# Kernel tuning notes

Measured on AMD Instinct MI355X. Metric: run time of the kernel, lower is better.

## Reference

```python
import jax, jax.numpy as jnp
import numpy as np

D_MODEL = 1024
NUM_SYMBOLS = 1024
NUM_VALUES = 1024
GRAPH_STEPS = 3
BATCH = 64


def setup_inputs() -> dict:
    key = jax.random.key(0)
    ks = jax.random.split(key, 12)
    B, S, V, D = BATCH, NUM_SYMBOLS, NUM_VALUES, D_MODEL
    scale = 0.02
    return {
        "map_memory": jax.random.normal(ks[0], (B, S, V), jnp.float32) * scale,
        "step_memory": jax.random.normal(ks[1], (B, S, S), jnp.float32) * scale,
        "query_idx": jax.random.randint(ks[2], (B,), 0, S),
        "query_mask": jnp.ones((B,), jnp.float32),
        "symbol_bank": jax.random.normal(ks[3], (S, D), jnp.float32) * scale,
        "value_bank": jax.random.normal(ks[4], (V, D), jnp.float32) * scale,
        "Wo1": jax.random.normal(ks[5], (D, D), jnp.float32) * scale,
        "bo1": jnp.zeros((D,), jnp.float32),
        "Wo2": jax.random.normal(ks[6], (D, V), jnp.float32) * scale,
        "bo2": jnp.zeros((V,), jnp.float32),
        "Wf1": jax.random.normal(ks[7], (D, D), jnp.float32) * scale,
        "bf1": jnp.zeros((D,), jnp.float32),
        "Wf2": jax.random.normal(ks[8], (D, D), jnp.float32) * scale,
        "bf2": jnp.zeros((D,), jnp.float32),
    }


def reference(map_memory, step_memory, query_idx, query_mask,
              symbol_bank, value_bank,
              Wo1, bo1, Wo2, bo2, Wf1, bf1, Wf2, bf2):
    # query_state: [B, S] one-hot masked
    query_state = jax.nn.one_hot(query_idx, NUM_SYMBOLS, dtype=jnp.float32)
    query_state = query_state * query_mask[:, None]

    acc_values = jnp.einsum('bs,bsv->bv', query_state, map_memory)   # [B, V]
    acc_symbols = jnp.einsum('bs,sd->bd', query_state, symbol_bank)  # [B, D]

    def walk_step(carry, _):
        walk, values, symbols = carry
        next_walk = jnp.einsum('bs,bst->bt', walk, step_memory)
        next_values = values + jnp.einsum('bs,bsv->bv', next_walk, map_memory)
        next_symbols = symbols + jnp.einsum('bs,sd->bd', next_walk, symbol_bank)
        return (next_walk, next_values, next_symbols), None

    (_, acc_values, acc_symbols), _ = jax.lax.scan(
        walk_step, (query_state, acc_values, acc_symbols), xs=None,
        length=GRAPH_STEPS)

    graph_state = acc_symbols + jnp.einsum('bv,vd->bd', acc_values, value_bank)

    logits = jax.nn.gelu(graph_state @ Wo1 + bo1) @ Wo2 + bo2      # [B, V]
    feedback = jax.nn.gelu(graph_state @ Wf1 + bf1) @ Wf2 + bf2    # [B, D]
    return logits, feedback
```

## Files before the change

### kernel.cpp

```cpp
#include <hip/hip_runtime.h>

#define BB 64
#define SS 1024
#define NN 1024
#define PARTS 16
#define KC 64

typedef float f4 __attribute__((ext_vector_type(4)));

template<int ASRC, int REV, int NT>
__global__ __launch_bounds__(256) void k_walkp(const float* __restrict__ A,
                                               const float* __restrict__ P,
                                               const float* __restrict__ W,
                                               float* __restrict__ Cp,
                                               const int* __restrict__ qidx,
                                               const float* __restrict__ qmask) {
    const int part = blockIdx.x;
    const int b    = REV ? (gridDim.y - 1 - blockIdx.y) : blockIdx.y;
    const int k0   = part * KC;

    __shared__ float As[KC];
    if (threadIdx.x < KC) {
        float v;
        if (ASRC == 0) {
            int q = qidx[b];
            v = qmask[b] * W[(size_t)b * SS * SS + (size_t)q * SS + k0 + threadIdx.x];
        } else if (ASRC == 1) {
            v = 0.f;
            #pragma unroll
            for (int p = 0; p < PARTS; ++p)
                v += P[(size_t)p * BB * SS + b * SS + k0 + threadIdx.x];
        } else {
            v = A[b * SS + k0 + threadIdx.x];
        }
        As[threadIdx.x] = v;
    }
    __syncthreads();

    const float* Wp = W + (size_t)b * SS * SS + (size_t)k0 * NN + threadIdx.x * 4;
    f4 acc = {0.f, 0.f, 0.f, 0.f};
    for (int k = 0; k < KC; ++k) {
        f4 wv;
        if (NT) wv = __builtin_nontemporal_load((const f4*)(Wp + (size_t)k * NN));
        else    wv = *(const f4*)(Wp + (size_t)k * NN);
        float a = As[k];
        acc.x = fmaf(a, wv.x, acc.x);
        acc.y = fmaf(a, wv.y, acc.y);
        acc.z = fmaf(a, wv.z, acc.z);
        acc.w = fmaf(a, wv.w, acc.w);
    }
    f4* c = (f4*)(Cp + (size_t)part * BB * SS + (size_t)b * SS) + threadIdx.x;
    *c = acc;
}

__global__ void k_wsum(const float* __restrict__ SM,
                       const float* __restrict__ P,
                       const int* __restrict__ qidx, const float* __restrict__ qmask,
                       float* __restrict__ Wsum) {
    int b = blockIdx.x;
    int q = qidx[b];
    float m = qmask[b];
    int s0 = threadIdx.x * 4;

    f4 acc = m * (*(const f4*)(SM + (size_t)b * SS * SS + (size_t)q * SS + s0));
    #pragma unroll
    for (int p = 0; p < 2 * PARTS; ++p)
        acc += *(const f4*)(P + (size_t)p * BB * SS + b * SS + s0);
    int d = q - s0;
    if (d >= 0 && d < 4) acc[d] += m;
    *(f4*)(Wsum + b * SS + s0) = acc;
}

template<int ROWS, int KCS, int AR0, int AR1>
__global__ __launch_bounds__(256) void k_small(const float* __restrict__ A0,
                                               const float* __restrict__ W0,
                                               float* __restrict__ C0,
                                               const float* __restrict__ A1,
                                               const float* __restrict__ W1,
                                               float* __restrict__ C1,
                                               const float* __restrict__ P) {
    const int   ar = blockIdx.z ? AR1 : AR0;
    const float* A = blockIdx.z ? A1 : A0;
    const float* W = blockIdx.z ? W1 : W0;
    float*       C = blockIdx.z ? C1 : C0;
    const int k0 = blockIdx.x * KCS;
    const int r0 = blockIdx.y * ROWS;

    __shared__ float As[ROWS * KCS];
    for (int i = threadIdx.x; i < ROWS * KCS; i += 256) {
        int r = i / KCS, k = i % KCS;
        float v;
        if (ar) {
            v = 0.f;
            #pragma unroll
            for (int p = 0; p < PARTS; ++p)
                v += P[(size_t)p * BB * SS + (size_t)(r0 + r) * SS + k0 + k];
        } else {
            v = A[(r0 + r) * NN + k0 + k];
        }
        As[i] = v;
    }
    __syncthreads();

    const float* Wp = W + (size_t)k0 * NN + threadIdx.x * 4;
    float acc[ROWS][4];
    #pragma unroll
    for (int r = 0; r < ROWS; ++r) {
        acc[r][0] = 0.f; acc[r][1] = 0.f; acc[r][2] = 0.f; acc[r][3] = 0.f;
    }
    for (int k = 0; k < KCS; ++k) {
        float4 wv = *(const float4*)(Wp + (size_t)k * NN);
        #pragma unroll
        for (int r = 0; r < ROWS; ++r) {
            float a = As[r * KCS + k];
            acc[r][0] = fmaf(a, wv.x, acc[r][0]);
            acc[r][1] = fmaf(a, wv.y, acc[r][1]);
            acc[r][2] = fmaf(a, wv.z, acc[r][2]);
            acc[r][3] = fmaf(a, wv.w, acc[r][3]);
        }
    }
    const int t = threadIdx.x * 4;
    #pragma unroll
    for (int r = 0; r < ROWS; ++r) {
        float* c = C + (size_t)(r0 + r) * NN + t;
        unsafeAtomicAdd(c + 0, acc[r][0]);
        unsafeAtomicAdd(c + 1, acc[r][1]);
        unsafeAtomicAdd(c + 2, acc[r][2]);
        unsafeAtomicAdd(c + 3, acc[r][3]);
    }
}

__global__ void k_biasgelu(float* __restrict__ h0, float* __restrict__ h1,
                           const float* __restrict__ b0, const float* __restrict__ b1) {
    float* h = blockIdx.y ? h1 : h0;
    const float* bias = blockIdx.y ? b1 : b0;
    int b = blockIdx.x;
    int t = threadIdx.x * 4;
    #pragma unroll
    for (int j = 0; j < 4; ++j) {
        int d = t + j;
        float x = h[b * NN + d] + bias[d];
        float c = 0.7978845608028654f * (x + 0.044715f * x * x * x);
        h[b * NN + d] = 0.5f * x * (1.0f + tanhf(c));
    }
}

__global__ void k_out(const float* __restrict__ lg, const float* __restrict__ fb,
                      const float* __restrict__ bo2, const float* __restrict__ bf2,
                      float* __restrict__ out) {
    int half = blockIdx.y;
    const float* src = half ? fb : lg;
    const float* bias = half ? bf2 : bo2;
    float* dst = out + (size_t)half * BB * NN;
    int b = blockIdx.x;
    int t = threadIdx.x * 4;
    #pragma unroll
    for (int j = 0; j < 4; ++j) {
        int n = t + j;
        dst[b * NN + n] = src[b * NN + n] + bias[n];
    }
}

extern "C" void kernel_launch(void* const* d_in, const int* in_sizes, int n_in,
                              void* d_out, int out_size, void* d_ws, size_t ws_size,
                              hipStream_t stream) {
    const float* MM   = (const float*)d_in[0];
    const float* SM   = (const float*)d_in[1];
    const int*   qidx = (const int*)d_in[2];
    const float* qmask= (const float*)d_in[3];
    const float* sb   = (const float*)d_in[4];
    const float* vb   = (const float*)d_in[5];
    const float* Wo1  = (const float*)d_in[6];
    const float* bo1  = (const float*)d_in[7];
    const float* Wo2  = (const float*)d_in[8];
    const float* bo2  = (const float*)d_in[9];
    const float* Wf1  = (const float*)d_in[10];
    const float* bf1  = (const float*)d_in[11];
    const float* Wf2  = (const float*)d_in[12];
    const float* bf2  = (const float*)d_in[13];
    float* out = (float*)d_out;

    float* ws = (float*)d_ws;
    float* pA   = ws;
    float* pB   = ws + 1048576;
    float* pC   = ws + 2097152;
    float* Wsum = ws + 3145728;
    float* gs   = ws + 3211264;
    float* h_o  = ws + 3276800;
    float* h_f  = ws + 3342336;
    float* lg   = ws + 3407872;
    float* fb   = ws + 3473408;

    hipMemsetAsync(gs, 0, 5 * 65536 * sizeof(float), stream);

    k_walkp<0, 0, 0><<<dim3(PARTS, BB), 256, 0, stream>>>(nullptr, nullptr, SM, pA, qidx, qmask);
    k_walkp<1, 1, 0><<<dim3(PARTS, BB), 256, 0, stream>>>(nullptr, pA, SM, pB, qidx, qmask);
    k_wsum<<<BB, 256, 0, stream>>>(SM, pA, qidx, qmask, Wsum);
    k_walkp<2, 0, 1><<<dim3(PARTS, BB), 256, 0, stream>>>(Wsum, nullptr, MM, pC, qidx, qmask);
    k_small<8, 128, 0, 1><<<dim3(8, 8, 2), 256, 0, stream>>>(Wsum, sb, gs, nullptr, vb, gs, pC);
    k_small<8, 128, 0, 0><<<dim3(8, 8, 2), 256, 0, stream>>>(gs, Wo1, h_o, gs, Wf1, h_f, nullptr);
    k_biasgelu<<<dim3(BB, 2), 256, 0, stream>>>(h_o, h_f, bo1, bf1);
    k_small<8, 128, 0, 0><<<dim3(8, 8, 2), 256, 0, stream>>>(h_o, Wo2, lg, h_f, Wf2, fb, nullptr);
    k_out<<<dim3(BB, 2), 256, 0, stream>>>(lg, fb, bo2, bf2, out);
}
```

Baseline: 754.5 us.

## Fuse bias-GELU and output bias into GEMM kernels, double split-K parts

```diff
diff --git a/kernel.cpp b/kernel.cpp
--- a/kernel.cpp
+++ b/kernel.cpp
@@ -3,8 +3,8 @@
 #define BB 64
 #define SS 1024
 #define NN 1024
-#define PARTS 16
-#define KC 64
+#define PARTS 32
+#define KC 32
 
 typedef float f4 __attribute__((ext_vector_type(4)));
 
@@ -39,6 +39,7 @@
 
     const float* Wp = W + (size_t)b * SS * SS + (size_t)k0 * NN + threadIdx.x * 4;
     f4 acc = {0.f, 0.f, 0.f, 0.f};
+    #pragma unroll 8
     for (int k = 0; k < KC; ++k) {
         f4 wv;
         if (NT) wv = __builtin_nontemporal_load((const f4*)(Wp + (size_t)k * NN));
@@ -71,18 +72,21 @@
     *(f4*)(Wsum + b * SS + s0) = acc;
 }
 
-template<int ROWS, int KCS, int AR0, int AR1>
+template<int ROWS, int KCS, int AR0, int AR1, int GELU>
 __global__ __launch_bounds__(256) void k_small(const float* __restrict__ A0,
                                                const float* __restrict__ W0,
                                                float* __restrict__ C0,
                                                const float* __restrict__ A1,
                                                const float* __restrict__ W1,
                                                float* __restrict__ C1,
-                                               const float* __restrict__ P) {
-    const int   ar = blockIdx.z ? AR1 : AR0;
-    const float* A = blockIdx.z ? A1 : A0;
-    const float* W = blockIdx.z ? W1 : W0;
-    float*       C = blockIdx.z ? C1 : C0;
+                                               const float* __restrict__ P,
+                                               const float* __restrict__ bias0,
+                                               const float* __restrict__ bias1) {
+    const int   ar  = blockIdx.z ? AR1 : AR0;
+    const float* A  = blockIdx.z ? A1 : A0;
+    const float* W  = blockIdx.z ? W1 : W0;
+    float*       C  = blockIdx.z ? C1 : C0;
+    const float* bi = blockIdx.z ? bias1 : bias0;
     const int k0 = blockIdx.x * KCS;
     const int r0 = blockIdx.y * ROWS;
 
@@ -98,6 +102,11 @@
         } else {
             v = A[(r0 + r) * NN + k0 + k];
         }
+        if (GELU) {
+            float x = v + bi[k0 + k];
+            float c = 0.7978845608028654f * (x + 0.044715f * x * x * x);
+            v = 0.5f * x * (1.0f + tanhf(c));
+        }
         As[i] = v;
     }
     __syncthreads();
@@ -108,6 +117,7 @@
     for (int r = 0; r < ROWS; ++r) {
         acc[r][0] = 0.f; acc[r][1] = 0.f; acc[r][2] = 0.f; acc[r][3] = 0.f;
     }
+    #pragma unroll 8
     for (int k = 0; k < KCS; ++k) {
         float4 wv = *(const float4*)(Wp + (size_t)k * NN);
         #pragma unroll
@@ -130,34 +140,18 @@
     }
 }
 
-__global__ void k_biasgelu(float* __restrict__ h0, float* __restrict__ h1,
-                           const float* __restrict__ b0, const float* __restrict__ b1) {
-    float* h = blockIdx.y ? h1 : h0;
-    const float* bias = blockIdx.y ? b1 : b0;
+__global__ void k_init(float* __restrict__ gs, float* __restrict__ h_o,
+                       float* __restrict__ h_f, float* __restrict__ out,
+                       const float* __restrict__ bo2, const float* __restrict__ bf2) {
     int b = blockIdx.x;
     int t = threadIdx.x * 4;
-    #pragma unroll
-    for (int j = 0; j < 4; ++j) {
-        int d = t + j;
-        float x = h[b * NN + d] + bias[d];
-        float c = 0.7978845608028654f * (x + 0.044715f * x * x * x);
-        h[b * NN + d] = 0.5f * x * (1.0f + tanhf(c));
-    }
-}
-
-__global__ void k_out(const float* __restrict__ lg, const float* __restrict__ fb,
-                      const float* __restrict__ bo2, const float* __restrict__ bf2,
-                      float* __restrict__ out) {
-    int half = blockIdx.y;
-    const float* src = half ? fb : lg;
-    const float* bias = half ? bf2 : bo2;
-    float* dst = out + (size_t)half * BB * NN;
-    int b = blockIdx.x;
-    int t = threadIdx.x * 4;
-    #pragma unroll
-    for (int j = 0; j < 4; ++j) {
-        int n = t + j;
-        dst[b * NN + n] = src[b * NN + n] + bias[n];
+    f4 z = {0.f, 0.f, 0.f, 0.f};
+    switch (blockIdx.y) {
+        case 0: *(f4*)(gs  + b * NN + t) = z; break;
+        case 1: *(f4*)(h_o + b * NN + t) = z; break;
+        case 2: *(f4*)(h_f + b * NN + t) = z; break;
+        case 3: *(f4*)(out + (size_t)b * NN + t) = *(const f4*)(bo2 + t); break;
+        case 4: *(f4*)(out + (size_t)(BB + b) * NN + t) = *(const f4*)(bf2 + t); break;
     }
 }
 
@@ -182,24 +176,23 @@
 
     float* ws = (float*)d_ws;
     float* pA   = ws;
-    float* pB   = ws + 1048576;
-    float* pC   = ws + 2097152;
-    float* Wsum = ws + 3145728;
-    float* gs   = ws + 3211264;
-    float* h_o  = ws + 3276800;
-    float* h_f  = ws + 3342336;
-    float* lg   = ws + 3407872;
-    float* fb   = ws + 3473408;
+    float* pB   = ws + 2097152;
+    float* pC   = ws + 4194304;
+    float* Wsum = ws + 6291456;
+    float* gs   = ws + 6356992;
+    float* h_o  = ws + 6422528;
+    float* h_f  = ws + 6488064;
 
-    hipMemsetAsync(gs, 0, 5 * 65536 * sizeof(float), stream);
+    k_init<<<dim3(BB, 5), 256, 0, stream>>>(gs, h_o, h_f, out, bo2, bf2);
 
     k_walkp<0, 0, 0><<<dim3(PARTS, BB), 256, 0, stream>>>(nullptr, nullptr, SM, pA, qidx, qmask);
     k_walkp<1, 1, 0><<<dim3(PARTS, BB), 256, 0, stream>>>(nullptr, pA, SM, pB, qidx, qmask);
     k_wsum<<<BB, 256, 0, stream>>>(SM, pA, qidx, qmask, Wsum);
     k_walkp<2, 0, 1><<<dim3(PARTS, BB), 256, 0, stream>>>(Wsum, nullptr, MM, pC, qidx, qmask);
-    k_small<8, 128, 0, 1><<<dim3(8, 8, 2), 256, 0, stream>>>(Wsum, sb, gs, nullptr, vb, gs, pC);
-    k_small<8, 128, 0, 0><<<dim3(8, 8, 2), 256, 0, stream>>>(gs, Wo1, h_o, gs, Wf1, h_f, nullptr);
-    k_biasgelu<<<dim3(BB, 2), 256, 0, stream>>>(h_o, h_f, bo1, bf1);
-    k_small<8, 128, 0, 0><<<dim3(8, 8, 2), 256, 0, stream>>>(h_o, Wo2, lg, h_f, Wf2, fb, nullptr);
-    k_out<<<dim3(BB, 2), 256, 0, stream>>>(lg, fb, bo2, bf2, out);
+    k_small<8, 64, 0, 1, 0><<<dim3(16, 8, 2), 256, 0, stream>>>(
+        Wsum, sb, gs, nullptr, vb, gs, pC, nullptr, nullptr);
+    k_small<8, 64, 0, 0, 0><<<dim3(16, 8, 2), 256, 0, stream>>>(
+        gs, Wo1, h_o, gs, Wf1, h_f, nullptr, nullptr, nullptr);
+    k_small<8, 64, 0, 0, 1><<<dim3(16, 8, 2), 256, 0, stream>>>(
+        h_o, Wo2, out, h_f, Wf2, out + (size_t)BB * NN, nullptr, bo1, bf1);
 }
```

Result: faster. 734.5 us (-2.7%).
